# Optimization experiments

Hardware: AMD Instinct MI355X
Metric: run time of the kernel (lower is better)

Reference implementation:

```python
import jax, jax.numpy as jnp
import numpy as np

N_NODES = 50000
N_EDGES = 1600000
F_IN = 128
NUM_CLASSES = 40


def _gat_conv(x, src, dst, W, a_src, a_dst, b, concat):
    # x: [N, Fin], W: [Fin, H*C], a_src/a_dst: [H, C], b: [H*C] or [C]
    H, C = a_src.shape
    N = x.shape[0]
    h = (x @ W).reshape(N, H, C)                       # [N,H,C]
    al_s = jnp.einsum('nhc,hc->nh', h, a_src)          # [N,H]
    al_d = jnp.einsum('nhc,hc->nh', h, a_dst)          # [N,H]
    e = jax.nn.leaky_relu(al_s[src] + al_d[dst], 0.2)  # [E,H]
    # segment softmax over destination nodes
    m = jax.ops.segment_max(e, dst, num_segments=N)    # [N,H]
    ex = jnp.exp(e - m[dst])
    s = jax.ops.segment_sum(ex, dst, num_segments=N)   # [N,H]
    alpha = ex / s[dst]                                # [E,H]
    out = jax.ops.segment_sum(h[src] * alpha[:, :, None], dst, num_segments=N)  # [N,H,C]
    if concat:
        return out.reshape(N, H * C) + b
    return out.mean(axis=1) + b


def setup_inputs() -> dict:
    key = jax.random.key(0)
    ks = jax.random.split(key, 12)
    s = 0.1
    inp = {
        'x': jax.random.normal(ks[0], (N_NODES, F_IN), jnp.float32),
        'edge_index': jax.random.randint(ks[1], (2, N_EDGES), 0, N_NODES, jnp.int64),
        # conv1: 128 -> 16, heads=4, concat
        'W1': jax.random.normal(ks[2], (F_IN, 4 * 16), jnp.float32) * s,
        'a1s': jax.random.normal(ks[3], (4, 16), jnp.float32) * s,
        'a1d': jax.random.normal(ks[4], (4, 16), jnp.float32) * s,
        'b1': jnp.zeros((4 * 16,), jnp.float32),
        # conv2: 64 -> 16, heads=4, concat
        'W2': jax.random.normal(ks[5], (64, 4 * 16), jnp.float32) * s,
        'a2s': jax.random.normal(ks[6], (4, 16), jnp.float32) * s,
        'a2d': jax.random.normal(ks[7], (4, 16), jnp.float32) * s,
        'b2': jnp.zeros((4 * 16,), jnp.float32),
        # conv3: 64 -> num_classes, heads=6, mean
        'W3': jax.random.normal(ks[8], (64, 6 * NUM_CLASSES), jnp.float32) * s,
        'a3s': jax.random.normal(ks[9], (6, NUM_CLASSES), jnp.float32) * s,
        'a3d': jax.random.normal(ks[10], (6, NUM_CLASSES), jnp.float32) * s,
        'b3': jnp.zeros((NUM_CLASSES,), jnp.float32),
    }
    return inp


def reference(x, edge_index, W1, a1s, a1d, b1, W2, a2s, a2d, b2, W3, a3s, a3d, b3):
    N = x.shape[0]
    loop = jnp.arange(N, dtype=edge_index.dtype)
    src = jnp.concatenate([edge_index[0], loop])  # add_self_loops=True (PyG default)
    dst = jnp.concatenate([edge_index[1], loop])
    h = jax.nn.elu(_gat_conv(x, src, dst, W1, a1s, a1d, b1, concat=True))
    h = jax.nn.elu(_gat_conv(h, src, dst, W2, a2s, a2d, b2, concat=True))
    h = jax.nn.elu(_gat_conv(h, src, dst, W3, a3s, a3d, b3, concat=False))
    return jax.nn.log_softmax(h, axis=1)
```

## Files before the change

kernel.cpp:

```cpp
#include <hip/hip_runtime.h>
#include <math.h>

#define N_NODES 50000
#define N_EDGES 1600000
#define NB      391
#define CHUNK   8192
#define NCHUNK  196

typedef __attribute__((ext_vector_type(2))) float v2f;
typedef __attribute__((ext_vector_type(4))) float f32x4;
typedef __attribute__((ext_vector_type(8))) __bf16 bf16x8;

__device__ __forceinline__ float lrelu02(float x) { return x > 0.f ? x : 0.2f * x; }
__device__ __forceinline__ float elu1(float x)    { return x > 0.f ? x : __expf(x) - 1.f; }

__device__ __forceinline__ unsigned short f2bf(float f) {
    unsigned int u = __float_as_uint(f);
    return (unsigned short)((u + 0x7fffu + ((u >> 16) & 1u)) >> 16);
}
__device__ __forceinline__ float bf2f(unsigned short s) {
    return __uint_as_float((unsigned int)s << 16);
}
__device__ __forceinline__ float2 bfp2(unsigned int u) {
    float2 r;
    r.x = __uint_as_float(u << 16);
    r.y = __uint_as_float(u & 0xffff0000u);
    return r;
}

union BF8U { unsigned short u[8]; bf16x8 v; };
__device__ __forceinline__ bf16x8 cvt8(float4 a, float4 b) {
    BF8U r;
    r.u[0] = f2bf(a.x); r.u[1] = f2bf(a.y); r.u[2] = f2bf(a.z); r.u[3] = f2bf(a.w);
    r.u[4] = f2bf(b.x); r.u[5] = f2bf(b.y); r.u[6] = f2bf(b.z); r.u[7] = f2bf(b.w);
    return r.v;
}

template<int FIN>
__global__ __launch_bounds__(256) void gemm_al_kernel(const float* __restrict__ x,
                               const float* __restrict__ W,
                               const float* __restrict__ a_s, const float* __restrict__ a_d,
                               unsigned short* __restrict__ h,
                               float* __restrict__ al_s, float* __restrict__ al_d) {
    constexpr int KS = FIN / 32;
    __shared__ alignas(16) unsigned short Wl[KS * 64 * 32];
    __shared__ alignas(16) unsigned short ot[64][64];
    const int tid = threadIdx.x;
    for (int i = tid; i < FIN * 64; i += 256) {
        int ks = i >> 11;
        int rem = i & 2047;
        int c = rem >> 5, r = rem & 31;
        Wl[i] = f2bf(W[(ks * 32 + r) * 64 + c]);
    }
    __syncthreads();

    const int wv = tid >> 6, l = tid & 63;
    const int m = l & 15, g = l >> 4;
    const int n0 = blockIdx.x * 64;
    int row = n0 + wv * 16 + m;
    if (row > N_NODES - 1) row = N_NODES - 1;
    const float* xr = x + (size_t)row * FIN + g * 8;

    f32x4 acc[4] = {};
#pragma unroll
    for (int ks = 0; ks < KS; ++ks) {
        float4 xa = *(const float4*)(xr + ks * 32);
        float4 xb = *(const float4*)(xr + ks * 32 + 4);
        bf16x8 af = cvt8(xa, xb);
        const unsigned short* wp = &Wl[ks * 2048 + g * 8];
#pragma unroll
        for (int t = 0; t < 4; ++t) {
            bf16x8 bf = *(const bf16x8*)(wp + (t * 16 + m) * 32);
            acc[t] = __builtin_amdgcn_mfma_f32_16x16x32_bf16(af, bf, acc[t], 0, 0, 0);
        }
    }
#pragma unroll
    for (int t = 0; t < 4; ++t)
#pragma unroll
        for (int j = 0; j < 4; ++j)
            ot[wv * 16 + g * 4 + j][t * 16 + m] = f2bf(acc[t][j]);
    __syncthreads();

    int vrows = N_NODES - n0; if (vrows > 64) vrows = 64;
    {
        unsigned int* ph = (unsigned int*)(h + (size_t)n0 * 64);
        for (int i = tid; i < vrows * 32; i += 256) {
            int r = i >> 5, c = i & 31;
            ph[i] = *(const unsigned int*)&ot[r][c * 2];
        }
    }
    {
        int node = tid >> 2, hd = tid & 3;
        if (node < vrows) {
            const float* as = a_s + hd * 16;
            const float* ad = a_d + hd * 16;
            float s1 = 0.f, s2 = 0.f;
#pragma unroll
            for (int c = 0; c < 16; c += 2) {
                unsigned int q = *(const unsigned int*)&ot[node][hd * 16 + c];
                float2 p = bfp2(q);
                s1 = fmaf(p.x, as[c], s1);     s2 = fmaf(p.x, ad[c], s2);
                s1 = fmaf(p.y, as[c + 1], s1); s2 = fmaf(p.y, ad[c + 1], s2);
            }
            al_s[(n0 + node) * 4 + hd] = s1;
            al_d[(n0 + node) * 4 + hd] = s2;
        }
    }
}

__global__ __launch_bounds__(256) void gemm80_kernel(const float* __restrict__ x,
                              const float* __restrict__ W,
                              const float* __restrict__ a_s, const float* __restrict__ a_d,
                              unsigned int* __restrict__ h8,
                              float* __restrict__ al_s, float* __restrict__ al_d) {
    __shared__ alignas(16) unsigned short Wl[2 * 80 * 32];
    __shared__ alignas(16) unsigned short ot[64][80];
    const int tid = threadIdx.x;
    const int nb = blockIdx.x / 3, third = blockIdx.x % 3;
    const int cb = third * 80;
    for (int i = tid; i < 2 * 80 * 32; i += 256) {
        int ks = i / 2560;
        int rem = i - ks * 2560;
        int c = rem >> 5, r = rem & 31;
        Wl[i] = f2bf(W[(ks * 32 + r) * 240 + cb + c]);
    }
    __syncthreads();

    const int wv = tid >> 6, l = tid & 63;
    const int m = l & 15, g = l >> 4;
    const int n0 = nb * 64;
    int row = n0 + wv * 16 + m;
    if (row > N_NODES - 1) row = N_NODES - 1;
    const float* xr = x + (size_t)row * 64 + g * 8;

    f32x4 acc[5] = {};
#pragma unroll
    for (int ks = 0; ks < 2; ++ks) {
        float4 xa = *(const float4*)(xr + ks * 32);
        float4 xb = *(const float4*)(xr + ks * 32 + 4);
        bf16x8 af = cvt8(xa, xb);
        const unsigned short* wp = &Wl[ks * 2560 + g * 8];
#pragma unroll
        for (int t = 0; t < 5; ++t) {
            bf16x8 bf = *(const bf16x8*)(wp + (t * 16 + m) * 32);
            acc[t] = __builtin_amdgcn_mfma_f32_16x16x32_bf16(af, bf, acc[t], 0, 0, 0);
        }
    }
#pragma unroll
    for (int t = 0; t < 5; ++t)
#pragma unroll
        for (int j = 0; j < 4; ++j)
            ot[wv * 16 + g * 4 + j][t * 16 + m] = f2bf(acc[t][j]);
    __syncthreads();

    int vrows = N_NODES - n0; if (vrows > 64) vrows = 64;
    {
        for (int i = tid; i < vrows * 20; i += 256) {
            int r = i / 20, c = i - r * 20;
            uint2 q = *(const uint2*)&ot[r][c * 4];
            float2 p0 = bfp2(q.x), p1 = bfp2(q.y);
            int lo = __builtin_amdgcn_cvt_pk_fp8_f32(p0.x, p0.y, 0, false);
            unsigned int packed = (unsigned int)__builtin_amdgcn_cvt_pk_fp8_f32(p1.x, p1.y, lo, true);
            h8[(size_t)(n0 + r) * 64 + cb / 4 + c] = packed;
        }
        if (third == 0) {
            for (int i = tid; i < vrows * 4; i += 256)
                h8[(size_t)(n0 + (i >> 2)) * 64 + 60 + (i & 3)] = 0;
        }
    }
    for (int t = tid; t < vrows * 2; t += 256) {
        int node = t >> 1, hh = t & 1;
        int hd = third * 2 + hh;
        const unsigned short* rp = &ot[node][hh * 40];
        const float* as = a_s + hd * 40;
        const float* ad = a_d + hd * 40;
        float s1 = 0.f, s2 = 0.f;
#pragma unroll
        for (int c = 0; c < 40; c += 2) {
            unsigned int q = *(const unsigned int*)(rp + c);
            float2 p = bfp2(q);
            s1 = fmaf(p.x, as[c], s1);     s2 = fmaf(p.x, ad[c], s2);
            s1 = fmaf(p.y, as[c + 1], s1); s2 = fmaf(p.y, ad[c + 1], s2);
        }
        al_s[(n0 + node) * 6 + hd] = s1;
        al_d[(n0 + node) * 6 + hd] = s2;
    }
}

__global__ __launch_bounds__(256) void bcnt_kernel(const int* __restrict__ ei, int* __restrict__ bcnt) {
    __shared__ int hist[NB];
    const int t = threadIdx.x;
    for (int i = t; i < NB; i += 256) hist[i] = 0;
    __syncthreads();
    const int e0 = blockIdx.x * CHUNK;
    int n = N_EDGES - e0; if (n > CHUNK) n = CHUNK;
    const int4* d4 = (const int4*)(ei + N_EDGES) + (e0 >> 2);
    for (int i = t; i < (n >> 2); i += 256) {
        int4 d = d4[i];
        atomicAdd(&hist[d.x >> 7], 1);
        atomicAdd(&hist[d.y >> 7], 1);
        atomicAdd(&hist[d.z >> 7], 1);
        atomicAdd(&hist[d.w >> 7], 1);
    }
    __syncthreads();
    for (int b = t; b < NB; b += 256)
        if (hist[b]) atomicAdd(&bcnt[b], hist[b]);
}

__global__ void scan391_kernel(const int* __restrict__ bcnt, int* __restrict__ bbase,
                               int* __restrict__ bcur) {
    __shared__ int wtot[8];
    int b = threadIdx.x;
    int lane = b & 63, w = b >> 6;
    int v = (b < NB) ? bcnt[b] : 0;
    int sc = v;
#pragma unroll
    for (int off = 1; off < 64; off <<= 1) {
        int u = __shfl_up(sc, off);
        if (lane >= off) sc += u;
    }
    if (lane == 63) wtot[w] = sc;
    __syncthreads();
    int add = 0;
    for (int k = 0; k < w; ++k) add += wtot[k];
    int excl = sc - v + add;
    if (b < NB) { bbase[b] = excl; bcur[b * 16] = excl; }
    if (b == 0) bbase[NB] = N_EDGES;
}

__global__ __launch_bounds__(256) void bucket2_kernel(const int* __restrict__ ei,
                                                      int* __restrict__ bcur,
                                                      unsigned int* __restrict__ stage) {
    __shared__ unsigned int vals[CHUNK];
    __shared__ int hist[NB];
    __shared__ int cnt2[NB];
    __shared__ int gbase[NB];
    const int t = threadIdx.x;
    for (int i = t; i < NB; i += 256) { hist[i] = 0; cnt2[i] = 0; }
    __syncthreads();
    const int e0 = blockIdx.x * CHUNK;
    int n = N_EDGES - e0; if (n > CHUNK) n = CHUNK;
    const int4* s4 = (const int4*)ei + (e0 >> 2);
    const int4* d4 = (const int4*)(ei + N_EDGES) + (e0 >> 2);
    for (int i = t; i < (n >> 2); i += 256) {
        int4 s = s4[i], d = d4[i];
        vals[4 * i + 0] = ((unsigned int)d.x << 16) | (unsigned int)s.x;
        vals[4 * i + 1] = ((unsigned int)d.y << 16) | (unsigned int)s.y;
        vals[4 * i + 2] = ((unsigned int)d.z << 16) | (unsigned int)s.z;
        vals[4 * i + 3] = ((unsigned int)d.w << 16) | (unsigned int)s.w;
        atomicAdd(&hist[d.x >> 7], 1);
        atomicAdd(&hist[d.y >> 7], 1);
        atomicAdd(&hist[d.z >> 7], 1);
        atomicAdd(&hist[d.w >> 7], 1);
    }
    __syncthreads();
    for (int b = t; b < NB; b += 256)
        if (hist[b]) gbase[b] = atomicAdd(&bcur[b * 16], hist[b]);
    __syncthreads();
    for (int i = t; i < n; i += 256) {
        unsigned int v = vals[i];
        int b = v >> 23;
        int r = atomicAdd(&cnt2[b], 1);
        stage[gbase[b] + r] = v & 0x7FFFFFu;
    }
}

__global__ __launch_bounds__(256) void place2_kernel(const unsigned int* __restrict__ stage,
                                                     const int* __restrict__ bbase,
                                                     int* __restrict__ rowptr,
                                                     unsigned short* __restrict__ csr) {
    __shared__ int hist[128];
    __shared__ int cur[128];
    __shared__ int wt[2];
    const int b = blockIdx.x;
    const int n0 = b * 128;
    const int t = threadIdx.x;
    const int base = bbase[b];
    const int endp = bbase[b + 1];
    if (t < 128) hist[t] = 0;
    __syncthreads();
    for (int i = base + t; i < endp; i += 256)
        atomicAdd(&hist[stage[i] >> 16], 1);
    __syncthreads();
    int v = 0, sc = 0;
    if (t < 128) {
        v = hist[t];
        int lane = t & 63, w = t >> 6;
        sc = v;
#pragma unroll
        for (int off = 1; off < 64; off <<= 1) {
            int u = __shfl_up(sc, off);
            if (lane >= off) sc += u;
        }
        if (lane == 63) wt[w] = sc;
    }
    __syncthreads();
    if (t < 128) {
        int add = (t >= 64) ? wt[0] : 0;
        int excl = sc - v + add;
        int n = n0 + t;
        if (n <= N_NODES) rowptr[n] = base + excl;
        cur[t] = base + excl;
    }
    __syncthreads();
    for (int i = base + t; i < endp; i += 256) {
        unsigned int e = stage[i];
        int pos = atomicAdd(&cur[e >> 16], 1);
        csr[pos] = (unsigned short)(e & 0xFFFFu);
    }
}

__global__ void agg64_kernel(const int* __restrict__ rowptr, const unsigned short* __restrict__ csr_src,
                             const float* __restrict__ al_s, const float* __restrict__ al_d,
                             const unsigned short* __restrict__ hb, const float* __restrict__ b,
                             float* __restrict__ xn) {
    int node = blockIdx.x * 4 + (threadIdx.x >> 6);
    int lane = threadIdx.x & 63;
    int half = lane >> 5;
    int hl = lane & 31;
    int c0 = hl * 2;
    int hd = hl >> 3;
    float ald = al_d[node * 4 + hd];
    int beg = rowptr[node], end = rowptr[node + 1];
    float denom = 0.f, a0 = 0.f, a1 = 0.f;
    if (half == 0) {
        float w = __expf(lrelu02(al_s[node * 4 + hd] + ald));
        float2 p = bfp2(*(const unsigned int*)(hb + (size_t)node * 64 + c0));
        denom = w; a0 = w * p.x; a1 = w * p.y;
    }
    int j = beg + half;
    for (; j + 6 < end; j += 8) {
        int s0 = csr_src[j], s1 = csr_src[j + 2], s2 = csr_src[j + 4], s3 = csr_src[j + 6];
        unsigned int q0 = *(const unsigned int*)(hb + (size_t)s0 * 64 + c0);
        unsigned int q1 = *(const unsigned int*)(hb + (size_t)s1 * 64 + c0);
        unsigned int q2 = *(const unsigned int*)(hb + (size_t)s2 * 64 + c0);
        unsigned int q3 = *(const unsigned int*)(hb + (size_t)s3 * 64 + c0);
        float w0 = __expf(lrelu02(al_s[s0 * 4 + hd] + ald));
        float w1 = __expf(lrelu02(al_s[s1 * 4 + hd] + ald));
        float w2 = __expf(lrelu02(al_s[s2 * 4 + hd] + ald));
        float w3 = __expf(lrelu02(al_s[s3 * 4 + hd] + ald));
        denom += (w0 + w1) + (w2 + w3);
        float2 p;
        p = bfp2(q0); a0 = fmaf(w0, p.x, a0); a1 = fmaf(w0, p.y, a1);
        p = bfp2(q1); a0 = fmaf(w1, p.x, a0); a1 = fmaf(w1, p.y, a1);
        p = bfp2(q2); a0 = fmaf(w2, p.x, a0); a1 = fmaf(w2, p.y, a1);
        p = bfp2(q3); a0 = fmaf(w3, p.x, a0); a1 = fmaf(w3, p.y, a1);
    }
    for (; j < end; j += 2) {
        int s0 = csr_src[j];
        unsigned int q0 = *(const unsigned int*)(hb + (size_t)s0 * 64 + c0);
        float w0 = __expf(lrelu02(al_s[s0 * 4 + hd] + ald));
        denom += w0;
        float2 p = bfp2(q0);
        a0 = fmaf(w0, p.x, a0); a1 = fmaf(w0, p.y, a1);
    }
    denom += __shfl_xor(denom, 32);
    a0 += __shfl_xor(a0, 32);
    a1 += __shfl_xor(a1, 32);
    if (half == 0) {
        float2 o;
        o.x = elu1(a0 / denom + b[c0]);
        o.y = elu1(a1 / denom + b[c0 + 1]);
        *(float2*)(xn + (size_t)node * 64 + c0) = o;
    }
}

__global__ void agg240_kernel(const int* __restrict__ rowptr, const unsigned short* __restrict__ csr_src,
                              const float* __restrict__ al_s, const float* __restrict__ al_d,
                              const unsigned int* __restrict__ h8, const float* __restrict__ b3,
                              float* __restrict__ y) {
    __shared__ float sh[4][240];
    int wv_id = threadIdx.x >> 6;
    int node = blockIdx.x * 4 + wv_id;
    int lane = threadIdx.x & 63;
    bool act = lane < 60;
    int c0 = lane * 4;
    int hd = act ? (c0 / 40) : 5;
    float ald = al_d[node * 6 + hd];
    int beg = rowptr[node], end = rowptr[node + 1];
    float w = __expf(lrelu02(al_s[node * 6 + hd] + ald));
    float denom = w;
    float4 acc;
    {
        unsigned int q = h8[(size_t)node * 64 + lane];
        v2f lo = __builtin_amdgcn_cvt_pk_f32_fp8((int)q, false);
        v2f hi = __builtin_amdgcn_cvt_pk_f32_fp8((int)q, true);
        acc.x = w * lo.x; acc.y = w * lo.y; acc.z = w * hi.x; acc.w = w * hi.y;
    }
    int j = beg;
    for (; j + 8 <= end; j += 8) {
        int s[8];
#pragma unroll
        for (int u = 0; u < 8; ++u) s[u] = csr_src[j + u];
        unsigned int q[8];
#pragma unroll
        for (int u = 0; u < 8; ++u) q[u] = h8[(size_t)s[u] * 64 + lane];
        float wvv[8];
#pragma unroll
        for (int u = 0; u < 8; ++u) wvv[u] = __expf(lrelu02(al_s[s[u] * 6 + hd] + ald));
#pragma unroll
        for (int u = 0; u < 8; ++u) {
            denom += wvv[u];
            v2f lo = __builtin_amdgcn_cvt_pk_f32_fp8((int)q[u], false);
            v2f hi = __builtin_amdgcn_cvt_pk_f32_fp8((int)q[u], true);
            acc.x = fmaf(wvv[u], lo.x, acc.x); acc.y = fmaf(wvv[u], lo.y, acc.y);
            acc.z = fmaf(wvv[u], hi.x, acc.z); acc.w = fmaf(wvv[u], hi.y, acc.w);
        }
    }
    for (; j < end; ++j) {
        int s0 = csr_src[j];
        unsigned int q0 = h8[(size_t)s0 * 64 + lane];
        float w0 = __expf(lrelu02(al_s[s0 * 6 + hd] + ald));
        denom += w0;
        v2f lo = __builtin_amdgcn_cvt_pk_f32_fp8((int)q0, false);
        v2f hi = __builtin_amdgcn_cvt_pk_f32_fp8((int)q0, true);
        acc.x = fmaf(w0, lo.x, acc.x); acc.y = fmaf(w0, lo.y, acc.y);
        acc.z = fmaf(w0, hi.x, acc.z); acc.w = fmaf(w0, hi.y, acc.w);
    }
    if (act) {
        float r = 1.f / denom;
        float* sp = &sh[wv_id][c0];
        sp[0] = acc.x * r; sp[1] = acc.y * r; sp[2] = acc.z * r; sp[3] = acc.w * r;
    }
    __syncthreads();
    float v;
    if (lane < 40) {
        const float* p = sh[wv_id];
        float s = 0.f;
#pragma unroll
        for (int hh = 0; hh < 6; ++hh) s += p[hh * 40 + lane];
        v = elu1(s * (1.f / 6.f) + b3[lane]);
    } else {
        v = -INFINITY;
    }
    float m = v;
#pragma unroll
    for (int o = 32; o > 0; o >>= 1) m = fmaxf(m, __shfl_xor(m, o));
    float ex = (lane < 40) ? __expf(v - m) : 0.f;
    float ssum = ex;
#pragma unroll
    for (int o = 32; o > 0; o >>= 1) ssum += __shfl_xor(ssum, o);
    if (lane < 40) y[(size_t)node * 40 + lane] = v - m - __logf(ssum);
}

extern "C" void kernel_launch(void* const* d_in, const int* in_sizes, int n_in,
                              void* d_out, int out_size, void* d_ws, size_t ws_size,
                              hipStream_t stream) {
    const float* x   = (const float*)d_in[0];
    const int*   ei  = (const int*)d_in[1];
    const float* W1  = (const float*)d_in[2];
    const float* a1s = (const float*)d_in[3];
    const float* a1d = (const float*)d_in[4];
    const float* b1  = (const float*)d_in[5];
    const float* W2  = (const float*)d_in[6];
    const float* a2s = (const float*)d_in[7];
    const float* a2d = (const float*)d_in[8];
    const float* b2  = (const float*)d_in[9];
    const float* W3  = (const float*)d_in[10];
    const float* a3s = (const float*)d_in[11];
    const float* a3d = (const float*)d_in[12];
    const float* b3  = (const float*)d_in[13];
    float* y = (float*)d_out;

    float* ws = (float*)d_ws;
    unsigned short* h_bf = (unsigned short*)ws;
    float* x_buf   = ws + 1600000;
    float* al_s    = ws + 4800000;
    float* al_d    = ws + 5100000;
    unsigned int* h8 = (unsigned int*)(ws + 5400000);
    int*   rowptr  = (int*)(ws + 8600000);
    unsigned short* csr_src = (unsigned short*)(ws + 8650008);
    unsigned int* stage = (unsigned int*)(ws + 9450008);
    int*   bcnt    = (int*)(ws + 11050008);
    int*   bbase   = (int*)(ws + 11050400);
    int*   bcur    = (int*)(ws + 11050792);

    hipMemsetAsync(bcnt, 0, NB * sizeof(int), stream);
    bcnt_kernel<<<NCHUNK, 256, 0, stream>>>(ei, bcnt);
    scan391_kernel<<<1, 512, 0, stream>>>(bcnt, bbase, bcur);
    bucket2_kernel<<<NCHUNK, 256, 0, stream>>>(ei, bcur, stage);
    place2_kernel<<<NB, 256, 0, stream>>>(stage, bbase, rowptr, csr_src);

    const int agg_grid = N_NODES / 4;
    const int gemm_gx = (N_NODES + 63) / 64;

    gemm_al_kernel<128><<<gemm_gx, 256, 0, stream>>>(x, W1, a1s, a1d, h_bf, al_s, al_d);
    agg64_kernel<<<agg_grid, 256, 0, stream>>>(rowptr, csr_src, al_s, al_d, h_bf, b1, x_buf);

    gemm_al_kernel<64><<<gemm_gx, 256, 0, stream>>>(x_buf, W2, a2s, a2d, h_bf, al_s, al_d);
    agg64_kernel<<<agg_grid, 256, 0, stream>>>(rowptr, csr_src, al_s, al_d, h_bf, b2, x_buf);

    gemm80_kernel<<<gemm_gx * 3, 256, 0, stream>>>(x_buf, W3, a3s, a3d, h8, al_s, al_d);
    agg240_kernel<<<agg_grid, 256, 0, stream>>>(rowptr, csr_src, al_s, al_d, h8, b3, y);
}
```

Baseline: 364.9 us.

## Widen per-lane gathers and split edges across lane groups in aggregation kernels

Both aggregation kernels are restructured so each lane loads 8 bytes per neighbor (4 bf16 or 8 fp8 values) and the wave is split into 4 (agg64) or 2 (agg240) edge groups that process interleaved neighbors, then reduced with cross-lane shuffles. This is meant to raise memory-level parallelism for the gather-bound neighbor loop and cut per-edge instruction count. Attention logits are prescaled by log2(e) in the GEMM kernels so the softmax can use the raw v_exp_f32 instruction, and leaky-relu becomes a branchless fmax. Addressing switches to 32-bit unsigned offsets. More shuffle reductions are added, and 32-bit offsets limit buffer size.

```diff
diff --git a/kernel.cpp b/kernel.cpp
--- a/kernel.cpp
+++ b/kernel.cpp
@@ -6,13 +6,17 @@
 #define NB      391
 #define CHUNK   8192
 #define NCHUNK  196
+#define LOG2E   1.44269504088896340736f
 
 typedef __attribute__((ext_vector_type(2))) float v2f;
 typedef __attribute__((ext_vector_type(4))) float f32x4;
 typedef __attribute__((ext_vector_type(8))) __bf16 bf16x8;
 
-__device__ __forceinline__ float lrelu02(float x) { return x > 0.f ? x : 0.2f * x; }
+__device__ __forceinline__ float lrelu02(float x) { return fmaxf(x, 0.2f * x); }
 __device__ __forceinline__ float elu1(float x)    { return x > 0.f ? x : __expf(x) - 1.f; }
+__device__ __forceinline__ float exp2_fast(float x) {
+    float r; asm("v_exp_f32 %0, %1" : "=v"(r) : "v"(x)); return r;
+}
 
 __device__ __forceinline__ unsigned short f2bf(float f) {
     unsigned int u = __float_as_uint(f);
@@ -102,8 +106,8 @@
                 s1 = fmaf(p.x, as[c], s1);     s2 = fmaf(p.x, ad[c], s2);
                 s1 = fmaf(p.y, as[c + 1], s1); s2 = fmaf(p.y, ad[c + 1], s2);
             }
-            al_s[(n0 + node) * 4 + hd] = s1;
-            al_d[(n0 + node) * 4 + hd] = s2;
+            al_s[(n0 + node) * 4 + hd] = s1 * LOG2E;
+            al_d[(n0 + node) * 4 + hd] = s2 * LOG2E;
         }
     }
 }
@@ -182,8 +186,8 @@
             s1 = fmaf(p.x, as[c], s1);     s2 = fmaf(p.x, ad[c], s2);
             s1 = fmaf(p.y, as[c + 1], s1); s2 = fmaf(p.y, ad[c + 1], s2);
         }
-        al_s[(n0 + node) * 6 + hd] = s1;
-        al_d[(n0 + node) * 6 + hd] = s2;
+        al_s[(n0 + node) * 6 + hd] = s1 * LOG2E;
+        al_d[(n0 + node) * 6 + hd] = s2 * LOG2E;
     }
 }
 
@@ -314,54 +318,67 @@
                              const float* __restrict__ al_s, const float* __restrict__ al_d,
                              const unsigned short* __restrict__ hb, const float* __restrict__ b,
                              float* __restrict__ xn) {
-    int node = blockIdx.x * 4 + (threadIdx.x >> 6);
-    int lane = threadIdx.x & 63;
-    int half = lane >> 5;
-    int hl = lane & 31;
-    int c0 = hl * 2;
-    int hd = hl >> 3;
-    float ald = al_d[node * 4 + hd];
-    int beg = rowptr[node], end = rowptr[node + 1];
-    float denom = 0.f, a0 = 0.f, a1 = 0.f;
-    if (half == 0) {
-        float w = __expf(lrelu02(al_s[node * 4 + hd] + ald));
-        float2 p = bfp2(*(const unsigned int*)(hb + (size_t)node * 64 + c0));
-        denom = w; a0 = w * p.x; a1 = w * p.y;
-    }
-    int j = beg + half;
-    for (; j + 6 < end; j += 8) {
-        int s0 = csr_src[j], s1 = csr_src[j + 2], s2 = csr_src[j + 4], s3 = csr_src[j + 6];
-        unsigned int q0 = *(const unsigned int*)(hb + (size_t)s0 * 64 + c0);
-        unsigned int q1 = *(const unsigned int*)(hb + (size_t)s1 * 64 + c0);
-        unsigned int q2 = *(const unsigned int*)(hb + (size_t)s2 * 64 + c0);
-        unsigned int q3 = *(const unsigned int*)(hb + (size_t)s3 * 64 + c0);
-        float w0 = __expf(lrelu02(al_s[s0 * 4 + hd] + ald));
-        float w1 = __expf(lrelu02(al_s[s1 * 4 + hd] + ald));
-        float w2 = __expf(lrelu02(al_s[s2 * 4 + hd] + ald));
-        float w3 = __expf(lrelu02(al_s[s3 * 4 + hd] + ald));
+    const int node = blockIdx.x * 4 + (threadIdx.x >> 6);
+    const int lane = threadIdx.x & 63;
+    const int eg = lane >> 4;
+    const int cl = lane & 15;
+    const int c0 = cl * 4;
+    const int hd = cl >> 2;
+    const float ald = al_d[(unsigned)(node * 4 + hd)];
+    const int beg = rowptr[node], end = rowptr[node + 1];
+    float denom = 0.f, a0 = 0.f, a1 = 0.f, a2 = 0.f, a3 = 0.f;
+    if (eg == 0) {
+        float w = exp2_fast(lrelu02(al_s[(unsigned)(node * 4 + hd)] + ald));
+        uint2 q = *(const uint2*)(hb + (unsigned)(node * 64 + c0));
+        float2 p0 = bfp2(q.x), p1 = bfp2(q.y);
+        denom = w;
+        a0 = w * p0.x; a1 = w * p0.y; a2 = w * p1.x; a3 = w * p1.y;
+    }
+    int j = beg + eg;
+    for (; j + 12 < end; j += 16) {
+        int s0 = csr_src[j], s1 = csr_src[j + 4], s2 = csr_src[j + 8], s3 = csr_src[j + 12];
+        uint2 q0 = *(const uint2*)(hb + (unsigned)(s0 * 64 + c0));
+        uint2 q1 = *(const uint2*)(hb + (unsigned)(s1 * 64 + c0));
+        uint2 q2 = *(const uint2*)(hb + (unsigned)(s2 * 64 + c0));
+        uint2 q3 = *(const uint2*)(hb + (unsigned)(s3 * 64 + c0));
+        float w0 = exp2_fast(lrelu02(al_s[(unsigned)(s0 * 4 + hd)] + ald));
+        float w1 = exp2_fast(lrelu02(al_s[(unsigned)(s1 * 4 + hd)] + ald));
+        float w2 = exp2_fast(lrelu02(al_s[(unsigned)(s2 * 4 + hd)] + ald));
+        float w3 = exp2_fast(lrelu02(al_s[(unsigned)(s3 * 4 + hd)] + ald));
         denom += (w0 + w1) + (w2 + w3);
         float2 p;
-        p = bfp2(q0); a0 = fmaf(w0, p.x, a0); a1 = fmaf(w0, p.y, a1);
-        p = bfp2(q1); a0 = fmaf(w1, p.x, a0); a1 = fmaf(w1, p.y, a1);
-        p = bfp2(q2); a0 = fmaf(w2, p.x, a0); a1 = fmaf(w2, p.y, a1);
-        p = bfp2(q3); a0 = fmaf(w3, p.x, a0); a1 = fmaf(w3, p.y, a1);
-    }
-    for (; j < end; j += 2) {
+        p = bfp2(q0.x); a0 = fmaf(w0, p.x, a0); a1 = fmaf(w0, p.y, a1);
+        p = bfp2(q0.y); a2 = fmaf(w0, p.x, a2); a3 = fmaf(w0, p.y, a3);
+        p = bfp2(q1.x); a0 = fmaf(w1, p.x, a0); a1 = fmaf(w1, p.y, a1);
+        p = bfp2(q1.y); a2 = fmaf(w1, p.x, a2); a3 = fmaf(w1, p.y, a3);
+        p = bfp2(q2.x); a0 = fmaf(w2, p.x, a0); a1 = fmaf(w2, p.y, a1);
+        p = bfp2(q2.y); a2 = fmaf(w2, p.x, a2); a3 = fmaf(w2, p.y, a3);
+        p = bfp2(q3.x); a0 = fmaf(w3, p.x, a0); a1 = fmaf(w3, p.y, a1);
+        p = bfp2(q3.y); a2 = fmaf(w3, p.x, a2); a3 = fmaf(w3, p.y, a3);
+    }
+    for (; j < end; j += 4) {
         int s0 = csr_src[j];
-        unsigned int q0 = *(const unsigned int*)(hb + (size_t)s0 * 64 + c0);
-        float w0 = __expf(lrelu02(al_s[s0 * 4 + hd] + ald));
+        uint2 q0 = *(const uint2*)(hb + (unsigned)(s0 * 64 + c0));
+        float w0 = exp2_fast(lrelu02(al_s[(unsigned)(s0 * 4 + hd)] + ald));
         denom += w0;
-        float2 p = bfp2(q0);
-        a0 = fmaf(w0, p.x, a0); a1 = fmaf(w0, p.y, a1);
-    }
-    denom += __shfl_xor(denom, 32);
-    a0 += __shfl_xor(a0, 32);
-    a1 += __shfl_xor(a1, 32);
-    if (half == 0) {
-        float2 o;
-        o.x = elu1(a0 / denom + b[c0]);
-        o.y = elu1(a1 / denom + b[c0 + 1]);
-        *(float2*)(xn + (size_t)node * 64 + c0) = o;
+        float2 p;
+        p = bfp2(q0.x); a0 = fmaf(w0, p.x, a0); a1 = fmaf(w0, p.y, a1);
+        p = bfp2(q0.y); a2 = fmaf(w0, p.x, a2); a3 = fmaf(w0, p.y, a3);
+    }
+    denom += __shfl_xor(denom, 16); denom += __shfl_xor(denom, 32);
+    a0 += __shfl_xor(a0, 16); a0 += __shfl_xor(a0, 32);
+    a1 += __shfl_xor(a1, 16); a1 += __shfl_xor(a1, 32);
+    a2 += __shfl_xor(a2, 16); a2 += __shfl_xor(a2, 32);
+    a3 += __shfl_xor(a3, 16); a3 += __shfl_xor(a3, 32);
+    if (lane < 16) {
+        float r = 1.f / denom;
+        float4 bv = *(const float4*)(b + c0);
+        float4 o;
+        o.x = elu1(fmaf(a0, r, bv.x));
+        o.y = elu1(fmaf(a1, r, bv.y));
+        o.z = elu1(fmaf(a2, r, bv.z));
+        o.w = elu1(fmaf(a3, r, bv.w));
+        *(float4*)(xn + (unsigned)(node * 64 + c0)) = o;
     }
 }
 
@@ -370,57 +387,62 @@
                               const unsigned int* __restrict__ h8, const float* __restrict__ b3,
                               float* __restrict__ y) {
     __shared__ float sh[4][240];
-    int wv_id = threadIdx.x >> 6;
-    int node = blockIdx.x * 4 + wv_id;
-    int lane = threadIdx.x & 63;
-    bool act = lane < 60;
-    int c0 = lane * 4;
-    int hd = act ? (c0 / 40) : 5;
-    float ald = al_d[node * 6 + hd];
-    int beg = rowptr[node], end = rowptr[node + 1];
-    float w = __expf(lrelu02(al_s[node * 6 + hd] + ald));
-    float denom = w;
-    float4 acc;
-    {
-        unsigned int q = h8[(size_t)node * 64 + lane];
-        v2f lo = __builtin_amdgcn_cvt_pk_f32_fp8((int)q, false);
-        v2f hi = __builtin_amdgcn_cvt_pk_f32_fp8((int)q, true);
-        acc.x = w * lo.x; acc.y = w * lo.y; acc.z = w * hi.x; acc.w = w * hi.y;
-    }
-    int j = beg;
-    for (; j + 8 <= end; j += 8) {
-        int s[8];
-#pragma unroll
-        for (int u = 0; u < 8; ++u) s[u] = csr_src[j + u];
-        unsigned int q[8];
-#pragma unroll
-        for (int u = 0; u < 8; ++u) q[u] = h8[(size_t)s[u] * 64 + lane];
-        float wvv[8];
-#pragma unroll
-        for (int u = 0; u < 8; ++u) wvv[u] = __expf(lrelu02(al_s[s[u] * 6 + hd] + ald));
-#pragma unroll
-        for (int u = 0; u < 8; ++u) {
-            denom += wvv[u];
-            v2f lo = __builtin_amdgcn_cvt_pk_f32_fp8((int)q[u], false);
-            v2f hi = __builtin_amdgcn_cvt_pk_f32_fp8((int)q[u], true);
-            acc.x = fmaf(wvv[u], lo.x, acc.x); acc.y = fmaf(wvv[u], lo.y, acc.y);
-            acc.z = fmaf(wvv[u], hi.x, acc.z); acc.w = fmaf(wvv[u], hi.y, acc.w);
-        }
-    }
-    for (; j < end; ++j) {
+    const int wv_id = threadIdx.x >> 6;
+    const int node = blockIdx.x * 4 + wv_id;
+    const int lane = threadIdx.x & 63;
+    const int eg = lane >> 5;
+    const int cl = lane & 31;
+    const int u0 = cl * 2;
+    int hd = cl / 5; if (hd > 5) hd = 5;
+    const float ald = al_d[(unsigned)(node * 6 + hd)];
+    const int beg = rowptr[node], end = rowptr[node + 1];
+    float denom = 0.f;
+    float acc[8] = {0.f, 0.f, 0.f, 0.f, 0.f, 0.f, 0.f, 0.f};
+    auto acc8 = [&](uint2 q, float w) {
+        v2f p0 = __builtin_amdgcn_cvt_pk_f32_fp8((int)q.x, false);
+        v2f p1 = __builtin_amdgcn_cvt_pk_f32_fp8((int)q.x, true);
+        v2f p2 = __builtin_amdgcn_cvt_pk_f32_fp8((int)q.y, false);
+        v2f p3 = __builtin_amdgcn_cvt_pk_f32_fp8((int)q.y, true);
+        acc[0] = fmaf(w, p0.x, acc[0]); acc[1] = fmaf(w, p0.y, acc[1]);
+        acc[2] = fmaf(w, p1.x, acc[2]); acc[3] = fmaf(w, p1.y, acc[3]);
+        acc[4] = fmaf(w, p2.x, acc[4]); acc[5] = fmaf(w, p2.y, acc[5]);
+        acc[6] = fmaf(w, p3.x, acc[6]); acc[7] = fmaf(w, p3.y, acc[7]);
+    };
+    if (eg == 0) {
+        float w = exp2_fast(lrelu02(al_s[(unsigned)(node * 6 + hd)] + ald));
+        uint2 q = *(const uint2*)(h8 + (unsigned)(node * 64) + u0);
+        denom = w;
+        acc8(q, w);
+    }
+    int j = beg + eg;
+    for (; j + 6 < end; j += 8) {
+        int s0 = csr_src[j], s1 = csr_src[j + 2], s2 = csr_src[j + 4], s3 = csr_src[j + 6];
+        uint2 q0 = *(const uint2*)(h8 + (unsigned)(s0 * 64) + u0);
+        uint2 q1 = *(const uint2*)(h8 + (unsigned)(s1 * 64) + u0);
+        uint2 q2 = *(const uint2*)(h8 + (unsigned)(s2 * 64) + u0);
+        uint2 q3 = *(const uint2*)(h8 + (unsigned)(s3 * 64) + u0);
+        float w0 = exp2_fast(lrelu02(al_s[(unsigned)(s0 * 6 + hd)] + ald));
+        float w1 = exp2_fast(lrelu02(al_s[(unsigned)(s1 * 6 + hd)] + ald));
+        float w2 = exp2_fast(lrelu02(al_s[(unsigned)(s2 * 6 + hd)] + ald));
+        float w3 = exp2_fast(lrelu02(al_s[(unsigned)(s3 * 6 + hd)] + ald));
+        denom += (w0 + w1) + (w2 + w3);
+        acc8(q0, w0); acc8(q1, w1); acc8(q2, w2); acc8(q3, w3);
+    }
+    for (; j < end; j += 2) {
         int s0 = csr_src[j];
-        unsigned int q0 = h8[(size_t)s0 * 64 + lane];
-        float w0 = __expf(lrelu02(al_s[s0 * 6 + hd] + ald));
+        uint2 q0 = *(const uint2*)(h8 + (unsigned)(s0 * 64) + u0);
+        float w0 = exp2_fast(lrelu02(al_s[(unsigned)(s0 * 6 + hd)] + ald));
         denom += w0;
-        v2f lo = __builtin_amdgcn_cvt_pk_f32_fp8((int)q0, false);
-        v2f hi = __builtin_amdgcn_cvt_pk_f32_fp8((int)q0, true);
-        acc.x = fmaf(w0, lo.x, acc.x); acc.y = fmaf(w0, lo.y, acc.y);
-        acc.z = fmaf(w0, hi.x, acc.z); acc.w = fmaf(w0, hi.y, acc.w);
-    }
-    if (act) {
+        acc8(q0, w0);
+    }
+    denom += __shfl_xor(denom, 32);
+#pragma unroll
+    for (int i = 0; i < 8; ++i) acc[i] += __shfl_xor(acc[i], 32);
+    if (eg == 0 && cl < 30) {
         float r = 1.f / denom;
-        float* sp = &sh[wv_id][c0];
-        sp[0] = acc.x * r; sp[1] = acc.y * r; sp[2] = acc.z * r; sp[3] = acc.w * r;
+        float* sp = &sh[wv_id][cl * 8];
+#pragma unroll
+        for (int i = 0; i < 8; ++i) sp[i] = acc[i] * r;
     }
     __syncthreads();
     float v;
```

Result: faster. 346.8 us (-4.9%).
